# Optimization experiments

Measured on AMD Instinct MI355X. Metric: run time of the kernel, lower is better.

The kernel has to match this reference:

```python
import jax, jax.numpy as jnp
import numpy as np
from jax import lax

B, H, N, F = 32, 168, 512, 8
P_STEPS = 24


def setup_inputs() -> dict:
    key = jax.random.key(0)
    ks = jax.random.split(key, 8)
    s = 0.02
    return {
        "x": jax.random.normal(ks[0], (B, H, N, F), dtype=jnp.float32),
        "conv_w": jax.random.normal(ks[1], (N * F, N), dtype=jnp.float32) * s,
        "conv_b": jnp.zeros((N,), dtype=jnp.float32),
        "lstm_k": jax.random.normal(ks[2], (N, 4 * N), dtype=jnp.float32) * s,
        "lstm_rk": jax.random.normal(ks[3], (N, 4 * N), dtype=jnp.float32) * s,
        "lstm_b": jnp.zeros((4 * N,), dtype=jnp.float32),
        "dense_w": jax.random.normal(ks[4], (N, N), dtype=jnp.float32) * s,
        "dense_b": jnp.zeros((N,), dtype=jnp.float32),
        "P": P_STEPS,
    }


def _lstm_cell(h, c, x_t, lstm_k, lstm_rk, lstm_b):
    # Keras LSTMCell gate order: i, f, g(candidate), o
    z = x_t @ lstm_k + h @ lstm_rk + lstm_b  # [B, 4N]
    i, f, g, o = jnp.split(z, 4, axis=-1)
    i = jax.nn.sigmoid(i)
    f = jax.nn.sigmoid(f)
    g = jnp.tanh(g)
    o = jax.nn.sigmoid(o)
    c_new = f * c + i * g
    h_new = o * jnp.tanh(c_new)
    return h_new, c_new


def reference(x, conv_w, conv_b, lstm_k, lstm_rk, lstm_b, dense_w, dense_b, P):
    b, hh, n, f = x.shape
    # Conv1D kernel_size=1 == per-timestep dense projection N*F -> N
    xr = x.reshape(b, hh, n * f) @ conv_w + conv_b  # [B, H, N]

    h0 = jnp.zeros((b, n), dtype=x.dtype)
    c0 = jnp.zeros((b, n), dtype=x.dtype)

    def enc_step(carry, x_t):
        h, c = carry
        h, c = _lstm_cell(h, c, x_t, lstm_k, lstm_rk, lstm_b)
        return (h, c), None

    (h, c), _ = lax.scan(enc_step, (h0, c0), xr.transpose(1, 0, 2))

    def dec_step(carry, _):
        h, c = carry
        h2, c2 = _lstm_cell(h, c, h, lstm_k, lstm_rk, lstm_b)
        return (h2, c2), h2

    _, preds = lax.scan(dec_step, (h, c), None, length=P)  # [P, B, N]
    preds = preds.transpose(1, 0, 2)  # [B, P, N]
    return preds @ dense_w + dense_b
```

## Files before the change

kernel.cpp:

```cpp
#include <hip/hip_runtime.h>
#include <hip/hip_bf16.h>
#include <math.h>

typedef __hip_bfloat16 bf16;
typedef __attribute__((ext_vector_type(8))) short short8;
typedef __attribute__((ext_vector_type(4))) float floatx4;

#define B_  32
#define H_  168
#define N_  512
#define P_  24
#define NF_ 4096
#define G4N 2048
#define M1  (B_*H_)
#define NX  (M1*NF_)
#define TSTEPS (H_+P_)
#define NWG 64
#define HSZ (B_*N_)

__global__ __launch_bounds__(256) void cvt_f32_bf16(const float* __restrict__ in,
                                                    bf16* __restrict__ out, int n4) {
  int i = blockIdx.x * 256 + threadIdx.x;
  if (i < n4) {
    float4 v = ((const float4*)in)[i];
    bf16 o[4] = {__float2bfloat16(v.x), __float2bfloat16(v.y),
                 __float2bfloat16(v.z), __float2bfloat16(v.w)};
    *(ulong1*)(out + (size_t)i * 4) = *(ulong1*)o;
  }
}

__global__ __launch_bounds__(256) void transpose_cvt(const float* __restrict__ in,
                                                     bf16* __restrict__ out,
                                                     int R, int C) {
  __shared__ float t[32][33];
  int bx = blockIdx.x, by = blockIdx.y;
  int tx = threadIdx.x, ty = threadIdx.y;
#pragma unroll
  for (int yy = 0; yy < 32; yy += 8)
    t[ty + yy][tx] = in[(size_t)(by * 32 + ty + yy) * C + bx * 32 + tx];
  __syncthreads();
#pragma unroll
  for (int yy = 0; yy < 32; yy += 8)
    out[(size_t)(bx * 32 + ty + yy) * R + by * 32 + tx] =
        __float2bfloat16(t[tx][ty + yy]);
}

__global__ __launch_bounds__(256) void transpose_add_cvt(const float* __restrict__ in1,
                                                         const float* __restrict__ in2,
                                                         bf16* __restrict__ out,
                                                         int R, int C) {
  __shared__ float t[32][33];
  int bx = blockIdx.x, by = blockIdx.y;
  int tx = threadIdx.x, ty = threadIdx.y;
#pragma unroll
  for (int yy = 0; yy < 32; yy += 8) {
    size_t idx = (size_t)(by * 32 + ty + yy) * C + bx * 32 + tx;
    t[ty + yy][tx] = in1[idx] + in2[idx];
  }
  __syncthreads();
#pragma unroll
  for (int yy = 0; yy < 32; yy += 8)
    out[(size_t)(bx * 32 + ty + yy) * R + by * 32 + tx] =
        __float2bfloat16(t[tx][ty + yy]);
}

template <bool OUT_BF16>
__global__ __launch_bounds__(256) void gemm_bt(const bf16* __restrict__ A,
                                               const bf16* __restrict__ BT,
                                               const float* __restrict__ bias,
                                               void* __restrict__ Cout,
                                               int M, int N, int K, int permute) {
  __shared__ short As[128 * 40];
  __shared__ short Bs[128 * 40];
  int tid  = threadIdx.x;
  int wave = tid >> 6, lane = tid & 63;
  int wm = wave >> 1, wn = wave & 1;
  int quad = lane >> 4, l16 = lane & 15;
  int m0 = blockIdx.y * 128, n0 = blockIdx.x * 128;

  floatx4 acc[4][4];
#pragma unroll
  for (int i = 0; i < 4; i++)
#pragma unroll
    for (int j = 0; j < 4; j++) acc[i][j] = (floatx4){0.f, 0.f, 0.f, 0.f};

  int r0 = tid >> 2;
  int c0 = (tid & 3) * 8;

  for (int k0 = 0; k0 < K; k0 += 32) {
    short8 a0 = *(const short8*)(A  + (size_t)(m0 + r0)      * K + k0 + c0);
    short8 a1 = *(const short8*)(A  + (size_t)(m0 + r0 + 64) * K + k0 + c0);
    short8 b0 = *(const short8*)(BT + (size_t)(n0 + r0)      * K + k0 + c0);
    short8 b1 = *(const short8*)(BT + (size_t)(n0 + r0 + 64) * K + k0 + c0);
    __syncthreads();
    *(short8*)(&As[r0 * 40 + c0])        = a0;
    *(short8*)(&As[(r0 + 64) * 40 + c0]) = a1;
    *(short8*)(&Bs[r0 * 40 + c0])        = b0;
    *(short8*)(&Bs[(r0 + 64) * 40 + c0]) = b1;
    __syncthreads();
    short8 af[4], bfr[4];
#pragma unroll
    for (int i = 0; i < 4; i++)
      af[i] = *(const short8*)(&As[(wm * 64 + i * 16 + l16) * 40 + quad * 8]);
#pragma unroll
    for (int j = 0; j < 4; j++)
      bfr[j] = *(const short8*)(&Bs[(wn * 64 + j * 16 + l16) * 40 + quad * 8]);
#pragma unroll
    for (int i = 0; i < 4; i++)
#pragma unroll
      for (int j = 0; j < 4; j++)
        acc[i][j] = __builtin_amdgcn_mfma_f32_16x16x32_bf16(af[i], bfr[j],
                                                            acc[i][j], 0, 0, 0);
  }
#pragma unroll
  for (int i = 0; i < 4; i++) {
    int row = m0 + wm * 64 + i * 16 + quad * 4;
#pragma unroll
    for (int j = 0; j < 4; j++) {
      int col = n0 + wn * 64 + j * 16 + l16;
      float bv = bias ? bias[col] : 0.f;
#pragma unroll
      for (int r = 0; r < 4; r++) {
        int gr = row + r;
        int orow = permute ? (gr % H_) * B_ + gr / H_ : gr;
        float v = acc[i][j][r] + bv;
        if (OUT_BF16)
          ((bf16*)Cout)[(size_t)orow * N + col] = __float2bfloat16(v);
        else
          ((float*)Cout)[(size_t)orow * N + col] = v;
      }
    }
  }
}

__global__ __launch_bounds__(256) void lstm_persist(
    const bf16* __restrict__ rkT,
    const bf16* __restrict__ wcT,
    const float* __restrict__ bvec,
    const float* __restrict__ xk,
    bf16* __restrict__ hring,
    bf16* __restrict__ preds,
    unsigned* __restrict__ bar) {
  __shared__ short Wenc[32][520];
  __shared__ short Wdec[32][520];
  __shared__ float zs[32][33];
  __shared__ bf16  hstage[32][8];

  int tid  = threadIdx.x;
  int wave = tid >> 6, lane = tid & 63;
  int tm = wave >> 1, tn = wave & 1;
  int quad = lane >> 4, l16 = lane & 15;
  int n0 = blockIdx.x * 8;
  int lc   = tn * 16 + l16;
  int gcol = ((lc >> 3) << 9) + n0 + (lc & 7);
  int brow = tm * 16 + quad * 4;

  for (int idx = tid; idx < 32 * 64; idx += 256) {
    int r = idx >> 6, ck = (idx & 63) << 3;
    int grow = ((r >> 3) << 9) + n0 + (r & 7);
    *(short8*)&Wenc[r][ck] = *(const short8*)(rkT + (size_t)grow * 512 + ck);
    *(short8*)&Wdec[r][ck] = *(const short8*)(wcT + (size_t)grow * 512 + ck);
  }
  float bias_r = bvec[gcol];
  int b = tid >> 3, j = tid & 7;
  int nn = n0 + j;
  float c_reg = 0.f;

  float xkv[4];
  {
    const float* xp = xk + (size_t)brow * G4N + gcol;
#pragma unroll
    for (int r = 0; r < 4; ++r) xkv[r] = xp[(size_t)r * G4N];
  }
  __syncthreads();

  for (int t = 0; t < TSTEPS; ++t) {
    const bf16* h_in  = hring + (size_t)t * HSZ;
    bf16*       h_out = hring + (size_t)(t + 1) * HSZ;
    const short(*Ws)[520] = (t < H_) ? Wenc : Wdec;

    float xn[4] = {0.f, 0.f, 0.f, 0.f};
    if (t + 1 < H_) {
      const float* xp = xk + (size_t)((t + 1) * B_ + brow) * G4N + gcol;
#pragma unroll
      for (int r = 0; r < 4; ++r) xn[r] = xp[(size_t)r * G4N];
    }

    floatx4 acc0 = (floatx4){0.f, 0.f, 0.f, 0.f};
    floatx4 acc1 = (floatx4){0.f, 0.f, 0.f, 0.f};
    const bf16*  ap = h_in + (size_t)(tm * 16 + l16) * 512 + quad * 8;
    const short* bp = &Ws[lc][quad * 8];
#pragma unroll
    for (int k0 = 0; k0 < 512; k0 += 64) {
      short8 av0 = *(const short8*)(ap + k0);
      short8 av1 = *(const short8*)(ap + k0 + 32);
      short8 bv0 = *(const short8*)(bp + k0);
      short8 bv1 = *(const short8*)(bp + k0 + 32);
      acc0 = __builtin_amdgcn_mfma_f32_16x16x32_bf16(av0, bv0, acc0, 0, 0, 0);
      acc1 = __builtin_amdgcn_mfma_f32_16x16x32_bf16(av1, bv1, acc1, 0, 0, 0);
    }
    floatx4 acc = acc0 + acc1;
#pragma unroll
    for (int r = 0; r < 4; ++r)
      zs[brow + r][lc] = acc[r] + bias_r + xkv[r];
    __syncthreads();

    float zi = zs[b][j], zf = zs[b][8 + j], zg = zs[b][16 + j], zo = zs[b][24 + j];
    float ig = 1.f / (1.f + __expf(-zi));
    float fg = 1.f / (1.f + __expf(-zf));
    float gg = tanhf(zg);
    float og = 1.f / (1.f + __expf(-zo));
    c_reg = fg * c_reg + ig * gg;
    float hn = og * tanhf(c_reg);
    hstage[b][j] = __float2bfloat16(hn);
    if (t >= H_)
      preds[(size_t)b * (P_ * N_) + (t - H_) * N_ + nn] = __float2bfloat16(hn);
    __syncthreads();

    if (tid < 64) {
      int bb = tid >> 1, f4 = (tid & 1) * 4;
      unsigned long long v = *(const unsigned long long*)&hstage[bb][f4];
      __hip_atomic_store((unsigned long long*)(h_out + bb * 512 + n0 + f4), v,
                         __ATOMIC_RELAXED, __HIP_MEMORY_SCOPE_AGENT);
    }
    __syncthreads();

    if (tid == 0) {
      unsigned old = __hip_atomic_fetch_add(&bar[t], 1u, __ATOMIC_RELAXED,
                                            __HIP_MEMORY_SCOPE_AGENT);
      if (old != NWG - 1) {
        while (__hip_atomic_load(&bar[t], __ATOMIC_RELAXED,
                                 __HIP_MEMORY_SCOPE_AGENT) < NWG)
          __builtin_amdgcn_s_sleep(1);
      }
    }
    __builtin_amdgcn_fence(__ATOMIC_ACQUIRE, "workgroup");
    __syncthreads();
#pragma unroll
    for (int r = 0; r < 4; ++r) xkv[r] = xn[r];
  }
}

extern "C" void kernel_launch(void* const* d_in, const int* in_sizes, int n_in,
                              void* d_out, int out_size, void* d_ws, size_t ws_size,
                              hipStream_t stream) {
  const float* x       = (const float*)d_in[0];
  const float* conv_w  = (const float*)d_in[1];
  const float* conv_b  = (const float*)d_in[2];
  const float* lstm_k  = (const float*)d_in[3];
  const float* lstm_rk = (const float*)d_in[4];
  const float* lstm_b  = (const float*)d_in[5];
  const float* dense_w = (const float*)d_in[6];
  const float* dense_b = (const float*)d_in[7];
  float* out = (float*)d_out;

  char* p = (char*)d_ws;
  auto carve = [&](size_t bytes) {
    char* r = p;
    p += (bytes + 255) & ~(size_t)255;
    return r;
  };
  bf16*  xb    = (bf16*)carve((size_t)NX * 2);
  bf16*  xr    = (bf16*)carve((size_t)M1 * N_ * 2);
  float* xk    = (float*)carve((size_t)M1 * G4N * 4);
  bf16*  cwT   = (bf16*)carve((size_t)N_ * NF_ * 2);
  bf16*  kT    = (bf16*)carve((size_t)G4N * N_ * 2);
  bf16*  rkT   = (bf16*)carve((size_t)G4N * N_ * 2);
  bf16*  wcT   = (bf16*)carve((size_t)G4N * N_ * 2);
  bf16*  dwT   = (bf16*)carve((size_t)N_ * N_ * 2);
  bf16*  preds = (bf16*)carve((size_t)B_ * P_ * N_ * 2);
  bf16*  hring = (bf16*)carve((size_t)(TSTEPS + 1) * HSZ * 2);
  unsigned* bar  = (unsigned*)carve((size_t)TSTEPS * 4);

  cvt_f32_bf16<<<(NX / 4 + 255) / 256, 256, 0, stream>>>(x, xb, NX / 4);
  dim3 tb(32, 8);
  transpose_cvt<<<dim3(N_ / 32, NF_ / 32), tb, 0, stream>>>(conv_w, cwT, NF_, N_);
  transpose_cvt<<<dim3(G4N / 32, N_ / 32), tb, 0, stream>>>(lstm_k, kT, N_, G4N);
  transpose_cvt<<<dim3(G4N / 32, N_ / 32), tb, 0, stream>>>(lstm_rk, rkT, N_, G4N);
  transpose_add_cvt<<<dim3(G4N / 32, N_ / 32), tb, 0, stream>>>(lstm_k, lstm_rk,
                                                                wcT, N_, G4N);
  transpose_cvt<<<dim3(N_ / 32, N_ / 32), tb, 0, stream>>>(dense_w, dwT, N_, N_);
  hipMemsetAsync(hring, 0, (size_t)HSZ * 2, stream);
  hipMemsetAsync(bar, 0, (size_t)TSTEPS * 4, stream);

  gemm_bt<true><<<dim3(N_ / 128, M1 / 128), 256, 0, stream>>>(xb, cwT, conv_b, xr,
                                                              M1, N_, NF_, 1);
  gemm_bt<false><<<dim3(G4N / 128, M1 / 128), 256, 0, stream>>>(xr, kT, nullptr,
                                                                xk, M1, G4N, N_, 0);

  lstm_persist<<<NWG, 256, 0, stream>>>(rkT, wcT, lstm_b, xk, hring, preds, bar);

  gemm_bt<false><<<dim3(N_ / 128, (B_ * P_) / 128), 256, 0, stream>>>(
      preds, dwT, dense_b, out, B_ * P_, N_, N_, 0);
}
```

Measured before the change: 1.038 ms.

## Halve persistent LSTM workgroups, give each 16 hidden units

The persistent recurrent kernel now runs on 32 workgroups instead of 64, and each one owns 16 hidden units (64 gate columns) rather than 8. Each wave issues twice as many MFMAs per step and reuses the loaded h fragment across two column tiles. The aim is to cut the cost of the per-step grid barrier, since fewer workgroups take part in the atomic arrive and spin, and to spread the redundant h loads over more work. In exchange each step does more serial compute per workgroup and uses about twice the LDS for resident weights.

Result: slower. 1.216 ms (+17.2%).

```diff
diff --git a/kernel.cpp b/kernel.cpp
--- a/kernel.cpp
+++ b/kernel.cpp
@@ -15,7 +15,7 @@
 #define M1  (B_*H_)
 #define NX  (M1*NF_)
 #define TSTEPS (H_+P_)
-#define NWG 64
+#define NWG 32
 #define HSZ (B_*N_)
 
 __global__ __launch_bounds__(256) void cvt_f32_bf16(const float* __restrict__ in,
@@ -141,36 +141,42 @@
     bf16* __restrict__ hring,
     bf16* __restrict__ preds,
     unsigned* __restrict__ bar) {
-  __shared__ short Wenc[32][520];
-  __shared__ short Wdec[32][520];
-  __shared__ float zs[32][33];
-  __shared__ bf16  hstage[32][8];
+  __shared__ short Wenc[64][520];
+  __shared__ short Wdec[64][520];
+  __shared__ float zs[32][65];
+  __shared__ bf16  hstage[32][16];
 
   int tid  = threadIdx.x;
   int wave = tid >> 6, lane = tid & 63;
   int tm = wave >> 1, tn = wave & 1;
   int quad = lane >> 4, l16 = lane & 15;
-  int n0 = blockIdx.x * 8;
-  int lc   = tn * 16 + l16;
-  int gcol = ((lc >> 3) << 9) + n0 + (lc & 7);
+  int n0 = blockIdx.x * 16;
+  int lc0 = tn * 32 + l16;
+  int lc1 = lc0 + 16;
+  int gcol0 = ((lc0 >> 4) << 9) + n0 + (lc0 & 15);
+  int gcol1 = ((lc1 >> 4) << 9) + n0 + (lc1 & 15);
   int brow = tm * 16 + quad * 4;
 
-  for (int idx = tid; idx < 32 * 64; idx += 256) {
+  for (int idx = tid; idx < 64 * 64; idx += 256) {
     int r = idx >> 6, ck = (idx & 63) << 3;
-    int grow = ((r >> 3) << 9) + n0 + (r & 7);
+    int grow = ((r >> 4) << 9) + n0 + (r & 15);
     *(short8*)&Wenc[r][ck] = *(const short8*)(rkT + (size_t)grow * 512 + ck);
     *(short8*)&Wdec[r][ck] = *(const short8*)(wcT + (size_t)grow * 512 + ck);
   }
-  float bias_r = bvec[gcol];
-  int b = tid >> 3, j = tid & 7;
-  int nn = n0 + j;
-  float c_reg = 0.f;
-
-  float xkv[4];
+  float bias0 = bvec[gcol0];
+  float bias1 = bvec[gcol1];
+  int b = tid >> 3, j2 = tid & 7;
+  int jj0 = j2 * 2;
+  float c_reg0 = 0.f, c_reg1 = 0.f;
+
+  float xkv0[4], xkv1[4];
   {
-    const float* xp = xk + (size_t)brow * G4N + gcol;
-#pragma unroll
-    for (int r = 0; r < 4; ++r) xkv[r] = xp[(size_t)r * G4N];
+    const float* xp = xk + (size_t)brow * G4N;
+#pragma unroll
+    for (int r = 0; r < 4; ++r) {
+      xkv0[r] = xp[(size_t)r * G4N + gcol0];
+      xkv1[r] = xp[(size_t)r * G4N + gcol1];
+    }
   }
   __syncthreads();
 
@@ -179,46 +185,76 @@
     bf16*       h_out = hring + (size_t)(t + 1) * HSZ;
     const short(*Ws)[520] = (t < H_) ? Wenc : Wdec;
 
-    float xn[4] = {0.f, 0.f, 0.f, 0.f};
+    float xn0[4] = {0.f, 0.f, 0.f, 0.f};
+    float xn1[4] = {0.f, 0.f, 0.f, 0.f};
     if (t + 1 < H_) {
-      const float* xp = xk + (size_t)((t + 1) * B_ + brow) * G4N + gcol;
-#pragma unroll
-      for (int r = 0; r < 4; ++r) xn[r] = xp[(size_t)r * G4N];
-    }
-
-    floatx4 acc0 = (floatx4){0.f, 0.f, 0.f, 0.f};
-    floatx4 acc1 = (floatx4){0.f, 0.f, 0.f, 0.f};
-    const bf16*  ap = h_in + (size_t)(tm * 16 + l16) * 512 + quad * 8;
-    const short* bp = &Ws[lc][quad * 8];
+      const float* xp = xk + (size_t)((t + 1) * B_ + brow) * G4N;
+#pragma unroll
+      for (int r = 0; r < 4; ++r) {
+        xn0[r] = xp[(size_t)r * G4N + gcol0];
+        xn1[r] = xp[(size_t)r * G4N + gcol1];
+      }
+    }
+
+    floatx4 a00 = (floatx4){0.f, 0.f, 0.f, 0.f};
+    floatx4 a10 = (floatx4){0.f, 0.f, 0.f, 0.f};
+    floatx4 a01 = (floatx4){0.f, 0.f, 0.f, 0.f};
+    floatx4 a11 = (floatx4){0.f, 0.f, 0.f, 0.f};
+    const bf16*  ap  = h_in + (size_t)(tm * 16 + l16) * 512 + quad * 8;
+    const short* bp0 = &Ws[lc0][quad * 8];
+    const short* bp1 = &Ws[lc1][quad * 8];
 #pragma unroll
     for (int k0 = 0; k0 < 512; k0 += 64) {
       short8 av0 = *(const short8*)(ap + k0);
       short8 av1 = *(const short8*)(ap + k0 + 32);
-      short8 bv0 = *(const short8*)(bp + k0);
-      short8 bv1 = *(const short8*)(bp + k0 + 32);
-      acc0 = __builtin_amdgcn_mfma_f32_16x16x32_bf16(av0, bv0, acc0, 0, 0, 0);
-      acc1 = __builtin_amdgcn_mfma_f32_16x16x32_bf16(av1, bv1, acc1, 0, 0, 0);
-    }
-    floatx4 acc = acc0 + acc1;
-#pragma unroll
-    for (int r = 0; r < 4; ++r)
-      zs[brow + r][lc] = acc[r] + bias_r + xkv[r];
-    __syncthreads();
-
-    float zi = zs[b][j], zf = zs[b][8 + j], zg = zs[b][16 + j], zo = zs[b][24 + j];
-    float ig = 1.f / (1.f + __expf(-zi));
-    float fg = 1.f / (1.f + __expf(-zf));
-    float gg = tanhf(zg);
-    float og = 1.f / (1.f + __expf(-zo));
-    c_reg = fg * c_reg + ig * gg;
-    float hn = og * tanhf(c_reg);
-    hstage[b][j] = __float2bfloat16(hn);
-    if (t >= H_)
-      preds[(size_t)b * (P_ * N_) + (t - H_) * N_ + nn] = __float2bfloat16(hn);
-    __syncthreads();
-
-    if (tid < 64) {
-      int bb = tid >> 1, f4 = (tid & 1) * 4;
+      short8 b00 = *(const short8*)(bp0 + k0);
+      short8 b01 = *(const short8*)(bp0 + k0 + 32);
+      short8 b10 = *(const short8*)(bp1 + k0);
+      short8 b11 = *(const short8*)(bp1 + k0 + 32);
+      a00 = __builtin_amdgcn_mfma_f32_16x16x32_bf16(av0, b00, a00, 0, 0, 0);
+      a01 = __builtin_amdgcn_mfma_f32_16x16x32_bf16(av1, b01, a01, 0, 0, 0);
+      a10 = __builtin_amdgcn_mfma_f32_16x16x32_bf16(av0, b10, a10, 0, 0, 0);
+      a11 = __builtin_amdgcn_mfma_f32_16x16x32_bf16(av1, b11, a11, 0, 0, 0);
+    }
+    floatx4 acc0 = a00 + a01;
+    floatx4 acc1 = a10 + a11;
+#pragma unroll
+    for (int r = 0; r < 4; ++r) {
+      zs[brow + r][lc0] = acc0[r] + bias0 + xkv0[r];
+      zs[brow + r][lc1] = acc1[r] + bias1 + xkv1[r];
+    }
+    __syncthreads();
+
+    {
+      float zi = zs[b][jj0],      zf = zs[b][16 + jj0],
+            zg = zs[b][32 + jj0], zo = zs[b][48 + jj0];
+      float ig = 1.f / (1.f + __expf(-zi));
+      float fg = 1.f / (1.f + __expf(-zf));
+      float gg = tanhf(zg);
+      float og = 1.f / (1.f + __expf(-zo));
+      c_reg0 = fg * c_reg0 + ig * gg;
+      float hn = og * tanhf(c_reg0);
+      hstage[b][jj0] = __float2bfloat16(hn);
+    }
+    {
+      float zi = zs[b][jj0 + 1],      zf = zs[b][16 + jj0 + 1],
+            zg = zs[b][32 + jj0 + 1], zo = zs[b][48 + jj0 + 1];
+      float ig = 1.f / (1.f + __expf(-zi));
+      float fg = 1.f / (1.f + __expf(-zf));
+      float gg = tanhf(zg);
+      float og = 1.f / (1.f + __expf(-zo));
+      c_reg1 = fg * c_reg1 + ig * gg;
+      float hn = og * tanhf(c_reg1);
+      hstage[b][jj0 + 1] = __float2bfloat16(hn);
+    }
+    if (t >= H_) {
+      unsigned pv = *(const unsigned*)&hstage[b][jj0];
+      *(unsigned*)&preds[(size_t)b * (P_ * N_) + (t - H_) * N_ + n0 + jj0] = pv;
+    }
+    __syncthreads();
+
+    if (tid < 128) {
+      int bb = tid >> 2, f4 = (tid & 3) * 4;
       unsigned long long v = *(const unsigned long long*)&hstage[bb][f4];
       __hip_atomic_store((unsigned long long*)(h_out + bb * 512 + n0 + f4), v,
                          __ATOMIC_RELAXED, __HIP_MEMORY_SCOPE_AGENT);
@@ -237,7 +273,7 @@
     __builtin_amdgcn_fence(__ATOMIC_ACQUIRE, "workgroup");
     __syncthreads();
 #pragma unroll
-    for (int r = 0; r < 4; ++r) xkv[r] = xn[r];
+    for (int r = 0; r < 4; ++r) { xkv0[r] = xn0[r]; xkv1[r] = xn1[r]; }
   }
 }
 
```

## Replace global barrier with sentinel-poisoned data-flow polling on hidden state

Applied to the files above, without the earlier changes.

Removes the per-step global atomic barrier across the 64 workgroups. Instead, the hidden-state ring is prefilled with 0xFF (NaN sentinel) and each wave polls its own A-fragment with relaxed atomic loads until no 16-bit lane holds the 0xFFFF sentinel, then feeds the fragments straight into the MFMAs. This drops two __syncthreads and the atomic counter round-trip per timestep, letting workgroups proceed as soon as their inputs arrive. The risks are a larger register footprint for the held fragments, a large memset of the whole ring, and correctness relying on a computed bf16 h never equalling 0xFFFF.

Measured after the change: 1.698 ms. 1.64x slower.

```diff
diff --git a/kernel.cpp b/kernel.cpp
--- a/kernel.cpp
+++ b/kernel.cpp
@@ -133,14 +133,19 @@
   }
 }
 
+__device__ __forceinline__ bool fresh8(unsigned long long v) {
+  return (v & ~(v + 0x0001000100010001ull) & 0x8000800080008000ull) == 0;
+}
+
+typedef union { unsigned long long q[2]; short8 s; } frag_u;
+
 __global__ __launch_bounds__(256) void lstm_persist(
     const bf16* __restrict__ rkT,
     const bf16* __restrict__ wcT,
     const float* __restrict__ bvec,
     const float* __restrict__ xk,
     bf16* __restrict__ hring,
-    bf16* __restrict__ preds,
-    unsigned* __restrict__ bar) {
+    bf16* __restrict__ preds) {
   __shared__ short Wenc[32][520];
   __shared__ short Wdec[32][520];
   __shared__ float zs[32][33];
@@ -186,18 +191,46 @@
       for (int r = 0; r < 4; ++r) xn[r] = xp[(size_t)r * G4N];
     }
 
+    const char* apb = (const char*)h_in +
+                      ((size_t)(tm * 16 + l16) * 512 + quad * 8) * 2;
+    unsigned long long u[8][4];
+#pragma unroll
+    for (int c = 0; c < 8; ++c)
+#pragma unroll
+      for (int q = 0; q < 4; ++q)
+        u[c][q] = __hip_atomic_load(
+            (const unsigned long long*)(apb + c * 128 + (q >> 1) * 64 +
+                                        (q & 1) * 8),
+            __ATOMIC_RELAXED, __HIP_MEMORY_SCOPE_AGENT);
+    for (;;) {
+      bool again = false;
+#pragma unroll
+      for (int c = 0; c < 8; ++c)
+#pragma unroll
+        for (int q = 0; q < 4; ++q)
+          if (!fresh8(u[c][q])) {
+            u[c][q] = __hip_atomic_load(
+                (const unsigned long long*)(apb + c * 128 + (q >> 1) * 64 +
+                                            (q & 1) * 8),
+                __ATOMIC_RELAXED, __HIP_MEMORY_SCOPE_AGENT);
+            again = true;
+          }
+      if (!again) break;
+      __builtin_amdgcn_s_sleep(1);
+    }
+
     floatx4 acc0 = (floatx4){0.f, 0.f, 0.f, 0.f};
     floatx4 acc1 = (floatx4){0.f, 0.f, 0.f, 0.f};
-    const bf16*  ap = h_in + (size_t)(tm * 16 + l16) * 512 + quad * 8;
     const short* bp = &Ws[lc][quad * 8];
 #pragma unroll
-    for (int k0 = 0; k0 < 512; k0 += 64) {
-      short8 av0 = *(const short8*)(ap + k0);
-      short8 av1 = *(const short8*)(ap + k0 + 32);
-      short8 bv0 = *(const short8*)(bp + k0);
-      short8 bv1 = *(const short8*)(bp + k0 + 32);
-      acc0 = __builtin_amdgcn_mfma_f32_16x16x32_bf16(av0, bv0, acc0, 0, 0, 0);
-      acc1 = __builtin_amdgcn_mfma_f32_16x16x32_bf16(av1, bv1, acc1, 0, 0, 0);
+    for (int c = 0; c < 8; ++c) {
+      frag_u f0, f1;
+      f0.q[0] = u[c][0]; f0.q[1] = u[c][1];
+      f1.q[0] = u[c][2]; f1.q[1] = u[c][3];
+      short8 bv0 = *(const short8*)(bp + c * 64);
+      short8 bv1 = *(const short8*)(bp + c * 64 + 32);
+      acc0 = __builtin_amdgcn_mfma_f32_16x16x32_bf16(f0.s, bv0, acc0, 0, 0, 0);
+      acc1 = __builtin_amdgcn_mfma_f32_16x16x32_bf16(f1.s, bv1, acc1, 0, 0, 0);
     }
     floatx4 acc = acc0 + acc1;
 #pragma unroll
@@ -223,19 +256,6 @@
       __hip_atomic_store((unsigned long long*)(h_out + bb * 512 + n0 + f4), v,
                          __ATOMIC_RELAXED, __HIP_MEMORY_SCOPE_AGENT);
     }
-    __syncthreads();
-
-    if (tid == 0) {
-      unsigned old = __hip_atomic_fetch_add(&bar[t], 1u, __ATOMIC_RELAXED,
-                                            __HIP_MEMORY_SCOPE_AGENT);
-      if (old != NWG - 1) {
-        while (__hip_atomic_load(&bar[t], __ATOMIC_RELAXED,
-                                 __HIP_MEMORY_SCOPE_AGENT) < NWG)
-          __builtin_amdgcn_s_sleep(1);
-      }
-    }
-    __builtin_amdgcn_fence(__ATOMIC_ACQUIRE, "workgroup");
-    __syncthreads();
 #pragma unroll
     for (int r = 0; r < 4; ++r) xkv[r] = xn[r];
   }
@@ -270,7 +290,6 @@
   bf16*  dwT   = (bf16*)carve((size_t)N_ * N_ * 2);
   bf16*  preds = (bf16*)carve((size_t)B_ * P_ * N_ * 2);
   bf16*  hring = (bf16*)carve((size_t)(TSTEPS + 1) * HSZ * 2);
-  unsigned* bar  = (unsigned*)carve((size_t)TSTEPS * 4);
 
   cvt_f32_bf16<<<(NX / 4 + 255) / 256, 256, 0, stream>>>(x, xb, NX / 4);
   dim3 tb(32, 8);
@@ -280,15 +299,15 @@
   transpose_add_cvt<<<dim3(G4N / 32, N_ / 32), tb, 0, stream>>>(lstm_k, lstm_rk,
                                                                 wcT, N_, G4N);
   transpose_cvt<<<dim3(N_ / 32, N_ / 32), tb, 0, stream>>>(dense_w, dwT, N_, N_);
+  hipMemsetAsync(hring, 0xFF, (size_t)(TSTEPS + 1) * HSZ * 2, stream);
   hipMemsetAsync(hring, 0, (size_t)HSZ * 2, stream);
-  hipMemsetAsync(bar, 0, (size_t)TSTEPS * 4, stream);
 
   gemm_bt<true><<<dim3(N_ / 128, M1 / 128), 256, 0, stream>>>(xb, cwT, conv_b, xr,
                                                               M1, N_, NF_, 1);
   gemm_bt<false><<<dim3(G4N / 128, M1 / 128), 256, 0, stream>>>(xr, kT, nullptr,
                                                                 xk, M1, G4N, N_, 0);
 
-  lstm_persist<<<NWG, 256, 0, stream>>>(rkT, wcT, lstm_b, xk, hring, preds, bar);
+  lstm_persist<<<NWG, 256, 0, stream>>>(rkT, wcT, lstm_b, xk, hring, preds);
 
   gemm_bt<false><<<dim3(N_ / 128, (B_ * P_) / 128), 256, 0, stream>>>(
       preds, dwT, dense_b, out, B_ * P_, N_, N_, 0);
```

## Remap LSTM gate columns per wave to drop intra-step block barriers

Applied to the files above, without the earlier changes.

Reorders the recurrent weight rows so that each wave's 16x16 MFMA output tile holds all four gates (i,f,g,o) for 4 batch rows by 4 hidden units. The gate nonlinearity can then run inside the wave using a per-wave shared scratch, with no workgroup barrier. Each lane writes its own bf16 h value straight to global with an atomic store, which removes the hstage staging and one extra __syncthreads per step. The grid barrier is also skipped on the final step. This cuts per-step synchronisation on the serial recurrence critical path, at the cost of more, smaller 2-byte global stores and reliance on manual s_waitcnt for LDS ordering within a wave.

Result: slower. 1.199 ms (+15.5%).

```diff
diff --git a/kernel.cpp b/kernel.cpp
--- a/kernel.cpp
+++ b/kernel.cpp
@@ -143,27 +143,27 @@
     unsigned* __restrict__ bar) {
   __shared__ short Wenc[32][520];
   __shared__ short Wdec[32][520];
-  __shared__ float zs[32][33];
-  __shared__ bf16  hstage[32][8];
+  __shared__ float zsw[4][16][20];
 
   int tid  = threadIdx.x;
   int wave = tid >> 6, lane = tid & 63;
   int tm = wave >> 1, tn = wave & 1;
   int quad = lane >> 4, l16 = lane & 15;
   int n0 = blockIdx.x * 8;
-  int lc   = tn * 16 + l16;
-  int gcol = ((lc >> 3) << 9) + n0 + (lc & 7);
+  int gcol = ((l16 >> 2) << 9) + n0 + tn * 4 + (l16 & 3);
   int brow = tm * 16 + quad * 4;
 
   for (int idx = tid; idx < 32 * 64; idx += 256) {
     int r = idx >> 6, ck = (idx & 63) << 3;
-    int grow = ((r >> 3) << 9) + n0 + (r & 7);
+    int grow = (((r & 15) >> 2) << 9) + n0 + ((r >> 4) << 2) + (r & 3);
     *(short8*)&Wenc[r][ck] = *(const short8*)(rkT + (size_t)grow * 512 + ck);
     *(short8*)&Wdec[r][ck] = *(const short8*)(wcT + (size_t)grow * 512 + ck);
   }
   float bias_r = bvec[gcol];
-  int b = tid >> 3, j = tid & 7;
-  int nn = n0 + j;
+  int bg = tm * 16 + quad * 4 + (l16 >> 2);
+  int ng = n0 + tn * 4 + (l16 & 3);
+  int bl = quad * 4 + (l16 >> 2);
+  int nn = l16 & 3;
   float c_reg = 0.f;
 
   float xkv[4];
@@ -189,7 +189,7 @@
     floatx4 acc0 = (floatx4){0.f, 0.f, 0.f, 0.f};
     floatx4 acc1 = (floatx4){0.f, 0.f, 0.f, 0.f};
     const bf16*  ap = h_in + (size_t)(tm * 16 + l16) * 512 + quad * 8;
-    const short* bp = &Ws[lc][quad * 8];
+    const short* bp = &Ws[tn * 16 + l16][quad * 8];
 #pragma unroll
     for (int k0 = 0; k0 < 512; k0 += 64) {
       short8 av0 = *(const short8*)(ap + k0);
@@ -202,40 +202,42 @@
     floatx4 acc = acc0 + acc1;
 #pragma unroll
     for (int r = 0; r < 4; ++r)
-      zs[brow + r][lc] = acc[r] + bias_r + xkv[r];
-    __syncthreads();
-
-    float zi = zs[b][j], zf = zs[b][8 + j], zg = zs[b][16 + j], zo = zs[b][24 + j];
+      zsw[wave][quad * 4 + r][l16] = acc[r] + bias_r + xkv[r];
+    asm volatile("s_waitcnt lgkmcnt(0)" ::: "memory");
+    float zi = zsw[wave][bl][nn];
+    float zf = zsw[wave][bl][4 + nn];
+    float zg = zsw[wave][bl][8 + nn];
+    float zo = zsw[wave][bl][12 + nn];
+
     float ig = 1.f / (1.f + __expf(-zi));
     float fg = 1.f / (1.f + __expf(-zf));
     float gg = tanhf(zg);
     float og = 1.f / (1.f + __expf(-zo));
     c_reg = fg * c_reg + ig * gg;
     float hn = og * tanhf(c_reg);
-    hstage[b][j] = __float2bfloat16(hn);
+    bf16 hv = __float2bfloat16(hn);
+    unsigned short hu = *(unsigned short*)&hv;
+    __hip_atomic_store((unsigned short*)h_out + (size_t)bg * 512 + ng, hu,
+                       __ATOMIC_RELAXED, __HIP_MEMORY_SCOPE_AGENT);
     if (t >= H_)
-      preds[(size_t)b * (P_ * N_) + (t - H_) * N_ + nn] = __float2bfloat16(hn);
+      preds[(size_t)bg * (P_ * N_) + (t - H_) * N_ + ng] = hv;
+
+    asm volatile("s_waitcnt vmcnt(0)" ::: "memory");
     __syncthreads();
 
-    if (tid < 64) {
-      int bb = tid >> 1, f4 = (tid & 1) * 4;
-      unsigned long long v = *(const unsigned long long*)&hstage[bb][f4];
-      __hip_atomic_store((unsigned long long*)(h_out + bb * 512 + n0 + f4), v,
-                         __ATOMIC_RELAXED, __HIP_MEMORY_SCOPE_AGENT);
-    }
-    __syncthreads();
-
-    if (tid == 0) {
-      unsigned old = __hip_atomic_fetch_add(&bar[t], 1u, __ATOMIC_RELAXED,
-                                            __HIP_MEMORY_SCOPE_AGENT);
-      if (old != NWG - 1) {
-        while (__hip_atomic_load(&bar[t], __ATOMIC_RELAXED,
-                                 __HIP_MEMORY_SCOPE_AGENT) < NWG)
-          __builtin_amdgcn_s_sleep(1);
+    if (t + 1 < TSTEPS) {
+      if (tid == 0) {
+        unsigned old = __hip_atomic_fetch_add(&bar[t], 1u, __ATOMIC_RELAXED,
+                                              __HIP_MEMORY_SCOPE_AGENT);
+        if (old != NWG - 1) {
+          while (__hip_atomic_load(&bar[t], __ATOMIC_RELAXED,
+                                   __HIP_MEMORY_SCOPE_AGENT) < NWG)
+            __builtin_amdgcn_s_sleep(1);
+        }
       }
-    }
-    __builtin_amdgcn_fence(__ATOMIC_ACQUIRE, "workgroup");
-    __syncthreads();
+      __builtin_amdgcn_fence(__ATOMIC_ACQUIRE, "workgroup");
+      __syncthreads();
+    }
 #pragma unroll
     for (int r = 0; r < 4; ++r) xkv[r] = xn[r];
   }
```
